# Kernel optimization log

Hardware: AMD Instinct MI355X
Metric: run time of the kernel (lower is better)

## Reference

```python
import jax, jax.numpy as jnp
import numpy as np

BATCH, SEQ, STATE, D_IN, D_OUT = 32, 8192, 128, 128, 128


def setup_inputs() -> dict:
    key = jax.random.key(0)
    k1, k2, k3, k4, k5 = jax.random.split(key, 5)
    A = jnp.tril(jax.random.normal(k1, (STATE, STATE), dtype=jnp.float32) * 0.01)
    B = jax.random.normal(k2, (STATE, D_IN), dtype=jnp.float32) * 0.01
    C = jax.random.normal(k3, (D_OUT, STATE), dtype=jnp.float32) * 0.01
    D = jax.random.normal(k4, (D_OUT, D_IN), dtype=jnp.float32) * 0.01
    u = jax.random.normal(k5, (BATCH, SEQ, D_IN), dtype=jnp.float32)
    return {"u": u, "A": A, "B": B, "C": C, "D": D}


def reference(u, A, B, C, D):
    # u: [b, L, d_in]; A: [S, S] (lower-tri); B: [S, d_in]; C: [d_out, S]; D: [d_out, d_in]
    S = A.shape[0]
    Bu = jnp.einsum('bld,sd->bls', u, B)                      # [b, L, S]
    I_minus_A = jnp.eye(S, dtype=u.dtype) - A                 # [S, S], lower-tri
    # Solve (I - A) x = Bu^T. The matrix is shared across batch and time, so
    # fold (b, L) into one rhs-column axis: one trsm instead of b batched solves.
    rhs = Bu.reshape(-1, S).T                                 # [S, b*L]
    x = jax.scipy.linalg.solve_triangular(I_minus_A, rhs, lower=True)  # [S, b*L]
    x_seq = x.T.reshape(Bu.shape)                             # [b, L, S]
    y = jnp.einsum('bls,os->blo', x_seq, C) + jnp.einsum('bld,od->blo', u, D)
    return y
```

## Files before the change

kernel.cpp:

```cpp
#include <hip/hip_runtime.h>
#include <stdint.h>

typedef __attribute__((ext_vector_type(8))) short bf16x8;
typedef __attribute__((ext_vector_type(4))) float f32x4;

static __device__ __forceinline__ uint16_t f2bf(float f) {
    uint32_t u;
    __builtin_memcpy(&u, &f, 4);
    return (uint16_t)((u + 0x7FFFu + ((u >> 16) & 1u)) >> 16);
}

__global__ __launch_bounds__(128) void k12_solve_makeM(const float* __restrict__ Ag,
                                                       const float* __restrict__ Bg,
                                                       const float* __restrict__ Cg,
                                                       const float* __restrict__ Dg,
                                                       uint16_t* __restrict__ Mfrag) {
    __shared__ float Ap[16 * 128];
    __shared__ float Bp[16 * 64];
    __shared__ float xT[64 * 128];

    const int tid = threadIdx.x;
    const int dl  = tid & 63;
    const int d   = blockIdx.x * 64 + dl;
    const int sw  = (dl & 7) << 2;
    float* xrow = &xT[dl * 128];

    for (int p = 0; p < 8; ++p) {
        __syncthreads();
        {
            const f32x4* src = reinterpret_cast<const f32x4*>(Ag + p * 2048);
            f32x4* dst = reinterpret_cast<f32x4*>(Ap);
#pragma unroll
            for (int i = 0; i < 4; ++i) dst[i * 128 + tid] = src[i * 128 + tid];
#pragma unroll
            for (int w = 0; w < 8; ++w) {
                int idx = w * 128 + tid;
                int row = idx >> 6, col = idx & 63;
                Bp[idx] = Bg[(p * 16 + row) * 128 + blockIdx.x * 64 + col];
            }
        }
        __syncthreads();

        if (tid < 64) {
            float base[16];
#pragma unroll
            for (int i = 0; i < 16; ++i) base[i] = 0.f;
            for (int q = 0; q < 4 * p; ++q) {
                f32x4 xv = *reinterpret_cast<const f32x4*>(xrow + ((q * 4) ^ sw));
#pragma unroll
                for (int i = 0; i < 16; ++i) {
                    f32x4 av = *reinterpret_cast<const f32x4*>(Ap + i * 128 + q * 4);
                    base[i] += av[0] * xv[0] + av[1] * xv[1] + av[2] * xv[2] + av[3] * xv[3];
                }
            }
            const int t0 = p * 16;
#pragma unroll
            for (int sl = 0; sl < 16; ++sl) {
                const int s = t0 + sl;
                const float* Ar = Ap + sl * 128;
                float acc = base[sl];
#pragma unroll
                for (int qq = 0; qq < (sl >> 2); ++qq) {
                    int tq = t0 + qq * 4;
                    f32x4 av = *reinterpret_cast<const f32x4*>(Ar + tq);
                    f32x4 xv = *reinterpret_cast<const f32x4*>(xrow + (tq ^ sw));
                    acc += av[0] * xv[0] + av[1] * xv[1] + av[2] * xv[2] + av[3] * xv[3];
                }
#pragma unroll
                for (int k = 0; k < (sl & 3); ++k) {
                    int t = t0 + (sl & ~3) + k;
                    acc += Ar[t] * xrow[t ^ sw];
                }
                float xs = (Bp[sl * 64 + dl] + acc) / (1.0f - Ar[s]);
                xrow[s ^ sw] = xs;
            }
        }
    }

    const int oh = tid >> 6;
    for (int ot = 0; ot < 8; ++ot) {
        __syncthreads();
        for (int w = tid; w < 2048; w += 128) {
            int rr = w >> 7;
            int cc = w & 127;
            int o  = (rr >> 3) * 64 + ot * 8 + (rr & 7);
            Ap[w] = Cg[o * 128 + cc];
        }
        __syncthreads();
        float macc[8];
#pragma unroll
        for (int r = 0; r < 8; ++r) macc[r] = 0.f;
        const float* Crow = Ap + oh * (8 * 128);
        for (int q = 0; q < 32; ++q) {
            f32x4 xv = *reinterpret_cast<const f32x4*>(xrow + ((q * 4) ^ sw));
#pragma unroll
            for (int r = 0; r < 8; ++r) {
                f32x4 cv = *reinterpret_cast<const f32x4*>(Crow + r * 128 + q * 4);
                macc[r] += cv[0] * xv[0] + cv[1] * xv[1] + cv[2] * xv[2] + cv[3] * xv[3];
            }
        }
#pragma unroll
        for (int r = 0; r < 8; ++r) {
            const int o = oh * 64 + ot * 8 + r;
            float m = macc[r] + Dg[o * 128 + d];
            const int c = o >> 4, n = o & 15;
            const int t = d >> 5, r2 = d & 31;
            const int half = r2 >> 3, j = r2 & 7;
            const int lane = half * 16 + n;
            const int f = c * 4 + t;
            Mfrag[(f * 64 + lane) * 8 + j] = f2bf(m);
        }
    }
}

__global__ __launch_bounds__(256, 4) void k3_gemm(const float* __restrict__ U,
                                                  const uint16_t* __restrict__ Mfrag,
                                                  float* __restrict__ Y) {
    __shared__ uint16_t Msh[16384];
    {
        const uint4* src = reinterpret_cast<const uint4*>(Mfrag);
        uint4* dst = reinterpret_cast<uint4*>(Msh);
#pragma unroll
        for (int i = 0; i < 8; ++i)
            dst[threadIdx.x + 256 * i] = src[threadIdx.x + 256 * i];
    }
    __syncthreads();

    const int lane = threadIdx.x & 63;
    const int wid  = threadIdx.x >> 6;
    const int urow = lane & 15;
    const int kh   = lane >> 4;

    const size_t wrow = (size_t)blockIdx.x * 256 + (size_t)wid * 64;
    const float* up = U + (wrow + urow) * 128 + kh * 8;

    f32x4 buf[8];
#pragma unroll
    for (int t = 0; t < 4; ++t) {
        buf[2 * t]     = *reinterpret_cast<const f32x4*>(up + t * 32);
        buf[2 * t + 1] = *reinterpret_cast<const f32x4*>(up + t * 32 + 4);
    }

#pragma unroll
    for (int it = 0; it < 4; ++it) {
        bf16x8 Afr[4];
#pragma unroll
        for (int t = 0; t < 4; ++t) {
            f32x4 lo = buf[2 * t], hi = buf[2 * t + 1];
            bf16x8 a;
#pragma unroll
            for (int j = 0; j < 4; ++j) {
                a[j]     = (short)f2bf(lo[j]);
                a[4 + j] = (short)f2bf(hi[j]);
            }
            Afr[t] = a;
        }
        if (it < 3) {
            const float* upn = up + (size_t)(it + 1) * 16 * 128;
#pragma unroll
            for (int t = 0; t < 4; ++t) {
                buf[2 * t]     = *reinterpret_cast<const f32x4*>(upn + t * 32);
                buf[2 * t + 1] = *reinterpret_cast<const f32x4*>(upn + t * 32 + 4);
            }
        }
        f32x4 acc[8] = {};
#pragma unroll
        for (int c = 0; c < 8; ++c)
#pragma unroll
            for (int t = 0; t < 4; ++t) {
                bf16x8 b = *reinterpret_cast<const bf16x8*>(Msh + ((c * 4 + t) * 64 + lane) * 8);
                acc[c] = __builtin_amdgcn_mfma_f32_16x16x32_bf16(b, Afr[t], acc[c], 0, 0, 0);
            }
        float* yp = Y + (wrow + it * 16 + urow) * 128 + kh * 4;
#pragma unroll
        for (int c = 0; c < 8; ++c)
            *reinterpret_cast<f32x4*>(yp + c * 16) = acc[c];
    }
}

extern "C" void kernel_launch(void* const* d_in, const int* in_sizes, int n_in,
                              void* d_out, int out_size, void* d_ws, size_t ws_size,
                              hipStream_t stream) {
    const float* u = (const float*)d_in[0];
    const float* A = (const float*)d_in[1];
    const float* B = (const float*)d_in[2];
    const float* C = (const float*)d_in[3];
    const float* D = (const float*)d_in[4];

    uint16_t* Mfrag = (uint16_t*)d_ws;
    float*    Y     = (float*)d_out;

    hipLaunchKernelGGL(k12_solve_makeM, dim3(2),    dim3(128), 0, stream, A, B, C, D, Mfrag);
    hipLaunchKernelGGL(k3_gemm,         dim3(1024), dim3(256), 0, stream, u, Mfrag, Y);
}
```

Before: 332.0 us.

## Invert diagonal blocks upfront and parallelize triangular solve across four waves

The setup kernel first inverts each 16x16 diagonal block of (I-A) into a shared-memory table. Each block step then becomes a parallel off-diagonal accumulation followed by a small matrix-vector multiply with the precomputed inverse, replacing the serial 16-step forward substitution. All four waves now take part in the solve and in the C*x projection instead of only one or two. The main GEMM kernel is unchanged. Since the setup kernel uses only two blocks, its latency sits on the critical path, and inverting the blocks changes floating-point rounding slightly.

```diff
diff --git a/kernel.cpp b/kernel.cpp
--- a/kernel.cpp
+++ b/kernel.cpp
@@ -10,106 +10,121 @@
     return (uint16_t)((u + 0x7FFFu + ((u >> 16) & 1u)) >> 16);
 }
 
-__global__ __launch_bounds__(128) void k12_solve_makeM(const float* __restrict__ Ag,
+__global__ __launch_bounds__(256) void k12_solve_makeM(const float* __restrict__ Ag,
                                                        const float* __restrict__ Bg,
                                                        const float* __restrict__ Cg,
                                                        const float* __restrict__ Dg,
                                                        uint16_t* __restrict__ Mfrag) {
-    __shared__ float Ap[16 * 128];
-    __shared__ float Bp[16 * 64];
     __shared__ float xT[64 * 128];
+    __shared__ float Ad[8 * 256];
+    __shared__ float Wb[8 * 256];
+    __shared__ float Sb[16 * 64];
 
     const int tid = threadIdx.x;
     const int dl  = tid & 63;
     const int d   = blockIdx.x * 64 + dl;
+    const int wu  = __builtin_amdgcn_readfirstlane(tid >> 6);
     const int sw  = (dl & 7) << 2;
     float* xrow = &xT[dl * 128];
 
+#pragma unroll
+    for (int t = 0; t < 8; ++t) {
+        int idx = t * 256 + tid;
+        int p = idx >> 8, i = (idx >> 4) & 15, j = idx & 15;
+        Ad[idx] = Ag[(p * 16 + i) * 128 + p * 16 + j];
+    }
+    __syncthreads();
+
+    if (tid < 128) {
+        const int p = tid >> 4, j = tid & 15;
+        const float* App = Ad + p * 256;
+        float rd[16];
+#pragma unroll
+        for (int i = 0; i < 16; ++i) rd[i] = 1.0f / (1.0f - App[i * 16 + i]);
+        float w[16];
+#pragma unroll
+        for (int i = 0; i < 16; ++i) {
+            float s = (i == j) ? 1.0f : 0.0f;
+#pragma unroll
+            for (int t = 0; t < i; ++t) s += App[i * 16 + t] * w[t];
+            w[i] = s * rd[i];
+        }
+#pragma unroll
+        for (int i = 0; i < 16; ++i) Wb[p * 256 + i * 16 + j] = w[i];
+    }
+    __syncthreads();
+
     for (int p = 0; p < 8; ++p) {
+        float bx0 = Bg[(p * 16 + wu     ) * 128 + d];
+        float bx1 = Bg[(p * 16 + wu +  4) * 128 + d];
+        float bx2 = Bg[(p * 16 + wu +  8) * 128 + d];
+        float bx3 = Bg[(p * 16 + wu + 12) * 128 + d];
+
+        const float* Ar = Ag + (p * 16 + wu) * 128;
+        float a0 = 0.f, a1 = 0.f, a2 = 0.f, a3 = 0.f;
+#pragma unroll 2
+        for (int qp = 0; qp < p; ++qp) {
+#pragma unroll
+            for (int qq = 0; qq < 4; ++qq) {
+                const int t0 = qp * 16 + qq * 4;
+                f32x4 xv = *reinterpret_cast<const f32x4*>(xrow + (t0 ^ sw));
+                f32x4 v0 = *reinterpret_cast<const f32x4*>(Ar + t0);
+                f32x4 v1 = *reinterpret_cast<const f32x4*>(Ar + 4 * 128 + t0);
+                f32x4 v2 = *reinterpret_cast<const f32x4*>(Ar + 8 * 128 + t0);
+                f32x4 v3 = *reinterpret_cast<const f32x4*>(Ar + 12 * 128 + t0);
+                a0 += v0[0] * xv[0] + v0[1] * xv[1] + v0[2] * xv[2] + v0[3] * xv[3];
+                a1 += v1[0] * xv[0] + v1[1] * xv[1] + v1[2] * xv[2] + v1[3] * xv[3];
+                a2 += v2[0] * xv[0] + v2[1] * xv[1] + v2[2] * xv[2] + v2[3] * xv[3];
+                a3 += v3[0] * xv[0] + v3[1] * xv[1] + v3[2] * xv[2] + v3[3] * xv[3];
+            }
+        }
+        Sb[(wu     ) * 64 + dl] = bx0 + a0;
+        Sb[(wu +  4) * 64 + dl] = bx1 + a1;
+        Sb[(wu +  8) * 64 + dl] = bx2 + a2;
+        Sb[(wu + 12) * 64 + dl] = bx3 + a3;
         __syncthreads();
-        {
-            const f32x4* src = reinterpret_cast<const f32x4*>(Ag + p * 2048);
-            f32x4* dst = reinterpret_cast<f32x4*>(Ap);
-#pragma unroll
-            for (int i = 0; i < 4; ++i) dst[i * 128 + tid] = src[i * 128 + tid];
-#pragma unroll
-            for (int w = 0; w < 8; ++w) {
-                int idx = w * 128 + tid;
-                int row = idx >> 6, col = idx & 63;
-                Bp[idx] = Bg[(p * 16 + row) * 128 + blockIdx.x * 64 + col];
-            }
+
+        float sv[16];
+#pragma unroll
+        for (int j = 0; j < 16; ++j) sv[j] = Sb[j * 64 + dl];
+#pragma unroll
+        for (int k = 0; k < 4; ++k) {
+            const int r = wu + 4 * k;
+            const float* Wr = Wb + p * 256 + r * 16;
+            float xs = 0.f;
+#pragma unroll
+            for (int j4 = 0; j4 < 4; ++j4) {
+                f32x4 wv = *reinterpret_cast<const f32x4*>(Wr + j4 * 4);
+                xs += wv[0] * sv[4 * j4] + wv[1] * sv[4 * j4 + 1]
+                    + wv[2] * sv[4 * j4 + 2] + wv[3] * sv[4 * j4 + 3];
+            }
+            xrow[(p * 16 + r) ^ sw] = xs;
         }
         __syncthreads();
-
-        if (tid < 64) {
-            float base[16];
-#pragma unroll
-            for (int i = 0; i < 16; ++i) base[i] = 0.f;
-            for (int q = 0; q < 4 * p; ++q) {
-                f32x4 xv = *reinterpret_cast<const f32x4*>(xrow + ((q * 4) ^ sw));
-#pragma unroll
-                for (int i = 0; i < 16; ++i) {
-                    f32x4 av = *reinterpret_cast<const f32x4*>(Ap + i * 128 + q * 4);
-                    base[i] += av[0] * xv[0] + av[1] * xv[1] + av[2] * xv[2] + av[3] * xv[3];
-                }
-            }
-            const int t0 = p * 16;
-#pragma unroll
-            for (int sl = 0; sl < 16; ++sl) {
-                const int s = t0 + sl;
-                const float* Ar = Ap + sl * 128;
-                float acc = base[sl];
-#pragma unroll
-                for (int qq = 0; qq < (sl >> 2); ++qq) {
-                    int tq = t0 + qq * 4;
-                    f32x4 av = *reinterpret_cast<const f32x4*>(Ar + tq);
-                    f32x4 xv = *reinterpret_cast<const f32x4*>(xrow + (tq ^ sw));
-                    acc += av[0] * xv[0] + av[1] * xv[1] + av[2] * xv[2] + av[3] * xv[3];
-                }
-#pragma unroll
-                for (int k = 0; k < (sl & 3); ++k) {
-                    int t = t0 + (sl & ~3) + k;
-                    acc += Ar[t] * xrow[t ^ sw];
-                }
-                float xs = (Bp[sl * 64 + dl] + acc) / (1.0f - Ar[s]);
-                xrow[s ^ sw] = xs;
-            }
-        }
-    }
-
-    const int oh = tid >> 6;
-    for (int ot = 0; ot < 8; ++ot) {
-        __syncthreads();
-        for (int w = tid; w < 2048; w += 128) {
-            int rr = w >> 7;
-            int cc = w & 127;
-            int o  = (rr >> 3) * 64 + ot * 8 + (rr & 7);
-            Ap[w] = Cg[o * 128 + cc];
-        }
-        __syncthreads();
-        float macc[8];
-#pragma unroll
-        for (int r = 0; r < 8; ++r) macc[r] = 0.f;
-        const float* Crow = Ap + oh * (8 * 128);
-        for (int q = 0; q < 32; ++q) {
-            f32x4 xv = *reinterpret_cast<const f32x4*>(xrow + ((q * 4) ^ sw));
-#pragma unroll
-            for (int r = 0; r < 8; ++r) {
-                f32x4 cv = *reinterpret_cast<const f32x4*>(Crow + r * 128 + q * 4);
-                macc[r] += cv[0] * xv[0] + cv[1] * xv[1] + cv[2] * xv[2] + cv[3] * xv[3];
-            }
-        }
-#pragma unroll
-        for (int r = 0; r < 8; ++r) {
-            const int o = oh * 64 + ot * 8 + r;
-            float m = macc[r] + Dg[o * 128 + d];
-            const int c = o >> 4, n = o & 15;
-            const int t = d >> 5, r2 = d & 31;
-            const int half = r2 >> 3, j = r2 & 7;
-            const int lane = half * 16 + n;
-            const int f = c * 4 + t;
-            Mfrag[(f * 64 + lane) * 8 + j] = f2bf(m);
-        }
+    }
+
+    float macc[32];
+#pragma unroll
+    for (int oo = 0; oo < 32; ++oo) macc[oo] = 0.f;
+    const float* Cbase = Cg + (size_t)wu * 32 * 128;
+    for (int q = 0; q < 32; ++q) {
+        f32x4 xv = *reinterpret_cast<const f32x4*>(xrow + ((q * 4) ^ sw));
+#pragma unroll
+        for (int oo = 0; oo < 32; ++oo) {
+            f32x4 cv = *reinterpret_cast<const f32x4*>(Cbase + oo * 128 + q * 4);
+            macc[oo] += cv[0] * xv[0] + cv[1] * xv[1] + cv[2] * xv[2] + cv[3] * xv[3];
+        }
+    }
+#pragma unroll
+    for (int oo = 0; oo < 32; ++oo) {
+        const int o = wu * 32 + oo;
+        float m = macc[oo] + Dg[o * 128 + d];
+        const int c = o >> 4, n = o & 15;
+        const int t = d >> 5, r2 = d & 31;
+        const int half = r2 >> 3, j = r2 & 7;
+        const int lane = half * 16 + n;
+        const int f = c * 4 + t;
+        Mfrag[(f * 64 + lane) * 8 + j] = f2bf(m);
     }
 }
 
@@ -190,6 +205,6 @@
     uint16_t* Mfrag = (uint16_t*)d_ws;
     float*    Y     = (float*)d_out;
 
-    hipLaunchKernelGGL(k12_solve_makeM, dim3(2),    dim3(128), 0, stream, A, B, C, D, Mfrag);
+    hipLaunchKernelGGL(k12_solve_makeM, dim3(2),    dim3(256), 0, stream, A, B, C, D, Mfrag);
     hipLaunchKernelGGL(k3_gemm,         dim3(1024), dim3(256), 0, stream, u, Mfrag, Y);
 }
```

Result: no change. 325.6 us (-1.9%).
